# Performance work log

Hardware: AMD Instinct MI355X
Metric: run time of the kernel (lower is better)

## Reference

```python
import jax, jax.numpy as jnp
import numpy as np

B, CIN, H, W = 8, 128, 64, 64
COUT, KH, KW = 128, 3, 3
STRIDE = (1, 1)
PAD = (1, 1)
DIL = (1, 1)
GROUPS = 1
OFFSET_GROUPS = 1

def _out_size(i, k, s, p, d):
    return (i + 2 * p - d * (k - 1) - 1) // s + 1

HO = _out_size(H, KH, STRIDE[0], PAD[0], DIL[0])
WO = _out_size(W, KW, STRIDE[1], PAD[1], DIL[1])


def setup_inputs() -> dict:
    key = jax.random.key(0)
    k1, k2, k3, k4 = jax.random.split(key, 4)
    x = jax.random.normal(k1, (B, CIN, H, W), jnp.float32)
    offset = jax.random.normal(k2, (B, 2 * OFFSET_GROUPS * KH * KW, HO, WO), jnp.float32)
    fan_in = (CIN // GROUPS) * KH * KW
    bound = 1.0 / np.sqrt(fan_in)
    weight = jax.random.uniform(k3, (COUT, CIN // GROUPS, KH, KW), jnp.float32, -bound, bound)
    bias = jax.random.uniform(k4, (COUT,), jnp.float32, -bound, bound)
    return {"x": x, "offset": offset, "weight": weight, "bias": bias}


def _deform_conv2d(x, offset, weight, bias):
    Bn, Cin, Hi, Wi = x.shape
    K = KH * KW
    Goff, Gw = OFFSET_GROUPS, GROUPS
    Cpg = Cin // Goff

    # base sampling positions (before learned offsets)
    ys = jnp.arange(HO, dtype=jnp.float32) * STRIDE[0] - PAD[0]  # [HO]
    xs = jnp.arange(WO, dtype=jnp.float32) * STRIDE[1] - PAD[1]  # [WO]
    base_y = jnp.repeat(jnp.arange(KH, dtype=jnp.float32) * DIL[0], KW)  # [K]
    base_x = jnp.tile(jnp.arange(KW, dtype=jnp.float32) * DIL[1], KH)    # [K]

    # offsets: channel layout is 2*(g*K + k) + {0: dy, 1: dx}
    off = offset.reshape(Bn, Goff, K, 2, HO, WO)
    py = base_y[None, None, :, None, None] + ys[None, None, None, :, None] + off[:, :, :, 0]  # [B,Goff,K,HO,WO]
    px = base_x[None, None, :, None, None] + xs[None, None, None, None, :] + off[:, :, :, 1]

    y0 = jnp.floor(py)
    x0 = jnp.floor(px)
    ly = py - y0  # fractional weights
    lx = px - x0

    xg = x.reshape(Bn, Goff, Cpg, Hi * Wi)

    def gather_one(img, lin):  # img [Cpg, H*W], lin [K,HO,WO] -> [Cpg,K,HO,WO]
        return img[:, lin]

    gather = jax.vmap(jax.vmap(gather_one))  # over B and Goff

    def corner(yi, xi, w):
        # zero-padding semantics: out-of-bounds corner contributes 0
        mask = (yi >= 0) & (yi < Hi) & (xi >= 0) & (xi < Wi)
        iy = jnp.clip(yi, 0, Hi - 1).astype(jnp.int32)
        ix = jnp.clip(xi, 0, Wi - 1).astype(jnp.int32)
        lin = iy * Wi + ix  # [B,Goff,K,HO,WO]
        wm = (w * mask.astype(x.dtype))[:, :, None]  # broadcast over channel axis
        return gather(xg, lin) * wm  # [B,Goff,Cpg,K,HO,WO]

    val = (corner(y0, x0, (1 - ly) * (1 - lx))
           + corner(y0, x0 + 1, (1 - ly) * lx)
           + corner(y0 + 1, x0, ly * (1 - lx))
           + corner(y0 + 1, x0 + 1, ly * lx))  # [B,Goff,Cpg,K,HO,WO]

    # grouped conv accumulate
    val = val.reshape(Bn, Gw, Cin // Gw, K, HO, WO)
    wg = weight.reshape(Gw, COUT // Gw, Cin // Gw, K)
    out = jnp.einsum('bgckhw,gock->bgohw', val, wg).reshape(Bn, COUT, HO, WO)
    return out + bias[None, :, None, None]


def reference(x, offset, weight, bias):
    return _deform_conv2d(x, offset, weight, bias)
```

## Files before the change

### kernel.cpp

```cpp
#include <hip/hip_runtime.h>

typedef unsigned int   u32;
typedef unsigned short u16;
typedef short bf16x8 __attribute__((ext_vector_type(8)));
typedef float f32x4  __attribute__((ext_vector_type(4)));

#define CIN   128
#define COUT  128
#define Hh    64
#define Ww    64
#define Bb    8
#define KPOS  9
#define KDIM  (CIN*KPOS)
#define NKSTEP 36
#define XT_ELEMS (Bb*Hh*Ww*CIN)

__device__ __forceinline__ float bflo(u32 u){ return __uint_as_float(u << 16); }
__device__ __forceinline__ float bfhi(u32 u){ return __uint_as_float(u & 0xffff0000u); }

__device__ __forceinline__ u32 packbf(float a, float b){
    u32 ua = __float_as_uint(a);
    u32 ub = __float_as_uint(b);
    ua += 0x7fffu + ((ua >> 16) & 1u);
    ub += 0x7fffu + ((ub >> 16) & 1u);
    return (ua >> 16) | (ub & 0xffff0000u);
}
__device__ __forceinline__ u16 tobf(float a){
    u32 ua = __float_as_uint(a);
    ua += 0x7fffu + ((ua >> 16) & 1u);
    return (u16)(ua >> 16);
}

__global__ __launch_bounds__(256) void k_transpose(const float* __restrict__ x,
                                                   u16* __restrict__ xT){
    __shared__ float tile[32*33];
    int bi = blockIdx.x;
    int st = bi & 127, ct = (bi >> 7) & 3, b = bi >> 9;
    int sb = st * 32, cb = ct * 32;
    int tid = threadIdx.x;

    int i = tid >> 5, j = tid & 31;
    const float* xp = x + ((size_t)(b*CIN + cb) * 4096) + sb;
#pragma unroll
    for (int rr = 0; rr < 4; ++rr){
        int ci = i + rr*8;
        tile[ci*33 + j] = xp[(size_t)ci*4096 + j];
    }
    __syncthreads();

    int ii = tid >> 4, jj = tid & 15;
    u32* outp = (u32*)xT + ((size_t)b*4096 + sb)*64 + (cb >> 1) + jj;
#pragma unroll
    for (int rr = 0; rr < 2; ++rr){
        int sl = ii + rr*16;
        float v0 = tile[(2*jj  )*33 + sl];
        float v1 = tile[(2*jj+1)*33 + sl];
        outp[(size_t)sl*64] = packbf(v0, v1);
    }
}

__global__ __launch_bounds__(256) void k_wprep(const float* __restrict__ w,
                                               u16* __restrict__ Wt){
    int gid = blockIdx.x*256 + threadIdx.x;
    int jf   = gid & 7;
    int lane = (gid >> 3) & 63;
    int mt   = (gid >> 9) & 7;
    int kt   = gid >> 12;
    int m  = mt*16 + (lane & 15);
    int kk = (lane >> 4)*8 + jf;
    int ck = kt*32 + kk;
    int kpos = ck >> 7;
    int cin  = ck & 127;
    Wt[gid] = tobf(w[((size_t)m*128 + cin)*9 + kpos]);
}

__global__ __launch_bounds__(256, 1)
void k_main(const float* __restrict__ off, const float* __restrict__ bias,
            const u16* __restrict__ xT, const u16* __restrict__ Wt,
            float* __restrict__ out){
    __shared__ u32 Vsm[128*20];

    int tid = threadIdx.x;
    int bi  = blockIdx.x;
    int b   = bi & 7;
    int t   = bi >> 3;
    int s0  = t * 128;

    int p  = tid >> 1, hf = tid & 1;
    int ho = (s0 + p) >> 6;
    int wo = p & 63;
    const u16* xb_base = xT + (size_t)b * (Hh*Ww*CIN);

    int lane = tid & 63, wave = tid >> 6;
    int wm = wave >> 1, wn = wave & 1;
    int quad = lane >> 4, l16 = lane & 15;

    f32x4 acc[4][4];
#pragma unroll
    for (int i = 0; i < 4; ++i)
#pragma unroll
        for (int j = 0; j < 4; ++j) acc[i][j] = {0.f, 0.f, 0.f, 0.f};

    int   aa[4] = {0,0,0,0};
    float wt[4] = {0.f,0.f,0.f,0.f};

    for (int ks = 0; ks < NKSTEP; ++ks){
        uint4 araw[4];
#pragma unroll
        for (int i = 0; i < 4; ++i)
            araw[i] = *(const uint4*)(Wt + (size_t)(((ks*8 + wm*4 + i)*64 + lane))*8);

        if ((ks & 3) == 0){
            int kpos = ks >> 2;
            int kh = kpos / 3, kw = kpos - kh*3;
            size_t ob = ((size_t)(b*18 + 2*kpos))*4096 + (s0 + p);
            float dy = off[ob];
            float dx = off[ob + 4096];
            float py = (float)(ho + kh - 1) + dy;
            float px = (float)(wo + kw - 1) + dx;
            float y0f = floorf(py), x0f = floorf(px);
            float ly = py - y0f, lx = px - x0f;
            int y0 = (int)y0f, x0 = (int)x0f;
            int y1 = y0 + 1,  x1 = x0 + 1;
            float my0 = (y0 >= 0 && y0 < Hh) ? 1.f : 0.f;
            float my1 = (y1 >= 0 && y1 < Hh) ? 1.f : 0.f;
            float mx0 = (x0 >= 0 && x0 < Ww) ? 1.f : 0.f;
            float mx1 = (x1 >= 0 && x1 < Ww) ? 1.f : 0.f;
            float omly = 1.f - ly, omlx = 1.f - lx;
            wt[0] = omly*omlx*my0*mx0;
            wt[1] = omly*lx  *my0*mx1;
            wt[2] = ly  *omlx*my1*mx0;
            wt[3] = ly  *lx  *my1*mx1;
            int cy0 = min(max(y0,0),Hh-1), cy1 = min(max(y1,0),Hh-1);
            int cx0 = min(max(x0,0),Ww-1), cx1 = min(max(x1,0),Ww-1);
            aa[0] = (cy0*Ww + cx0)*CIN;
            aa[1] = (cy0*Ww + cx1)*CIN;
            aa[2] = (cy1*Ww + cx0)*CIN;
            aa[3] = (cy1*Ww + cx1)*CIN;
        }

        int coff = ((ks & 3) << 5) + hf*16;
        const u16* xb = xb_base + coff;
        uint4 q[4][2];
#pragma unroll
        for (int c = 0; c < 4; ++c){
            q[c][0] = *(const uint4*)(xb + aa[c]);
            q[c][1] = *(const uint4*)(xb + aa[c] + 8);
        }
        u32 res[8];
#pragma unroll
        for (int d = 0; d < 8; ++d){
            float lo = 0.f, hi = 0.f;
#pragma unroll
            for (int c = 0; c < 4; ++c){
                u32 u = ((const u32*)&q[c][0])[d];
                lo = fmaf(wt[c], bflo(u), lo);
                hi = fmaf(wt[c], bfhi(u), hi);
            }
            res[d] = packbf(lo, hi);
        }

        __syncthreads();
        u32* vrow = &Vsm[p*20 + hf*8];
        *(uint4*)(vrow    ) = *(uint4*)&res[0];
        *(uint4*)(vrow + 4) = *(uint4*)&res[4];
        __syncthreads();

        uint4 braw[4];
#pragma unroll
        for (int j = 0; j < 4; ++j)
            braw[j] = *(const uint4*)&Vsm[((wn*4 + j)*16 + l16)*20 + quad*4];
#pragma unroll
        for (int i = 0; i < 4; ++i){
            bf16x8 av = __builtin_bit_cast(bf16x8, araw[i]);
#pragma unroll
            for (int j = 0; j < 4; ++j){
                bf16x8 bv = __builtin_bit_cast(bf16x8, braw[j]);
                acc[i][j] = __builtin_amdgcn_mfma_f32_16x16x32_bf16(av, bv, acc[i][j], 0, 0, 0);
            }
        }
    }

#pragma unroll
    for (int i = 0; i < 4; ++i){
        int cout0 = (wm*4 + i)*16 + quad*4;
#pragma unroll
        for (int j = 0; j < 4; ++j){
            int pcol = (wn*4 + j)*16 + l16;
            size_t obase = ((size_t)(b*COUT + cout0))*4096 + (s0 + pcol);
#pragma unroll
            for (int r = 0; r < 4; ++r){
                out[obase + (size_t)r*4096] = acc[i][j][r] + bias[cout0 + r];
            }
        }
    }
}

extern "C" void kernel_launch(void* const* d_in, const int* in_sizes, int n_in,
                              void* d_out, int out_size, void* d_ws, size_t ws_size,
                              hipStream_t stream){
    const float* x    = (const float*)d_in[0];
    const float* off  = (const float*)d_in[1];
    const float* w    = (const float*)d_in[2];
    const float* bias = (const float*)d_in[3];
    float* out = (float*)d_out;

    u16* xT = (u16*)d_ws;
    u16* Wt = xT + XT_ELEMS;

    k_transpose<<<dim3(4096), dim3(256), 0, stream>>>(x, xT);
    k_wprep    <<<dim3(576),  dim3(256), 0, stream>>>(w, Wt);
    k_main     <<<dim3(256),  dim3(256), 0, stream>>>(off, bias, xT, Wt, out);
}
```

Before: 122.0 us.

## Halve spatial tile, double-buffer LDS, and prefetch next k-step gather

The main kernel now processes 64 output pixels per block instead of 128, which doubles the grid to 512 blocks and relaxes launch bounds to allow two blocks per CU. The im2col LDS buffer is double-buffered, and the next k-step's offset state, bilinear gather and weight fragments are loaded before the current step's MFMAs. This removes one barrier per step. The goal is better occupancy across the 256 CUs and overlap of gather latency with matrix math. In exchange, each block does half the MFMA work per weight-fragment load, so weight traffic from L2 doubles, and register pressure rises.

```diff
diff --git a/kernel.cpp b/kernel.cpp
--- a/kernel.cpp
+++ b/kernel.cpp
@@ -74,119 +74,137 @@
     Wt[gid] = tobf(w[((size_t)m*128 + cin)*9 + kpos]);
 }
 
-__global__ __launch_bounds__(256, 1)
+__global__ __launch_bounds__(256, 2)
 void k_main(const float* __restrict__ off, const float* __restrict__ bias,
             const u16* __restrict__ xT, const u16* __restrict__ Wt,
             float* __restrict__ out){
-    __shared__ u32 Vsm[128*20];
+    __shared__ u32 Vsm[2][64*20];
 
     int tid = threadIdx.x;
     int bi  = blockIdx.x;
     int b   = bi & 7;
     int t   = bi >> 3;
-    int s0  = t * 128;
-
-    int p  = tid >> 1, hf = tid & 1;
-    int ho = (s0 + p) >> 6;
-    int wo = p & 63;
+    int s0  = t * 64;
+
+    int p  = tid >> 2, qt = tid & 3;
+    int ho = t;
+    int wo = p;
     const u16* xb_base = xT + (size_t)b * (Hh*Ww*CIN);
 
     int lane = tid & 63, wave = tid >> 6;
     int wm = wave >> 1, wn = wave & 1;
     int quad = lane >> 4, l16 = lane & 15;
 
-    f32x4 acc[4][4];
+    f32x4 acc[4][2];
 #pragma unroll
     for (int i = 0; i < 4; ++i)
 #pragma unroll
-        for (int j = 0; j < 4; ++j) acc[i][j] = {0.f, 0.f, 0.f, 0.f};
-
-    int   aa[4] = {0,0,0,0};
-    float wt[4] = {0.f,0.f,0.f,0.f};
-
-    for (int ks = 0; ks < NKSTEP; ++ks){
-        uint4 araw[4];
+        for (int j = 0; j < 2; ++j) acc[i][j] = {0.f, 0.f, 0.f, 0.f};
+
+    int   aa[4];
+    float wt[4];
+
+    auto state = [&](int kpos){
+        int kh = kpos / 3, kw = kpos - kh*3;
+        size_t ob = ((size_t)(b*18 + 2*kpos))*4096 + (s0 + p);
+        float dy = off[ob];
+        float dx = off[ob + 4096];
+        float py = (float)(ho + kh - 1) + dy;
+        float px = (float)(wo + kw - 1) + dx;
+        float y0f = floorf(py), x0f = floorf(px);
+        float ly = py - y0f, lx = px - x0f;
+        int y0 = (int)y0f, x0 = (int)x0f;
+        int y1 = y0 + 1,  x1 = x0 + 1;
+        float my0 = (y0 >= 0 && y0 < Hh) ? 1.f : 0.f;
+        float my1 = (y1 >= 0 && y1 < Hh) ? 1.f : 0.f;
+        float mx0 = (x0 >= 0 && x0 < Ww) ? 1.f : 0.f;
+        float mx1 = (x1 >= 0 && x1 < Ww) ? 1.f : 0.f;
+        float omly = 1.f - ly, omlx = 1.f - lx;
+        wt[0] = omly*omlx*my0*mx0;
+        wt[1] = omly*lx  *my0*mx1;
+        wt[2] = ly  *omlx*my1*mx0;
+        wt[3] = ly  *lx  *my1*mx1;
+        int cy0 = min(max(y0,0),Hh-1), cy1 = min(max(y1,0),Hh-1);
+        int cx0 = min(max(x0,0),Ww-1), cx1 = min(max(x1,0),Ww-1);
+        aa[0] = (cy0*Ww + cx0)*CIN;
+        aa[1] = (cy0*Ww + cx1)*CIN;
+        aa[2] = (cy1*Ww + cx0)*CIN;
+        aa[3] = (cy1*Ww + cx1)*CIN;
+    };
+
+    auto gather = [&](int ks, uint4 q[4]){
+        int coff = ((ks & 3) << 5) + qt*8;
+        const u16* xb = xb_base + coff;
+#pragma unroll
+        for (int c = 0; c < 4; ++c)
+            q[c] = *(const uint4*)(xb + aa[c]);
+    };
+
+    auto loadA = [&](int ks, uint4 a[4]){
 #pragma unroll
         for (int i = 0; i < 4; ++i)
-            araw[i] = *(const uint4*)(Wt + (size_t)(((ks*8 + wm*4 + i)*64 + lane))*8);
-
-        if ((ks & 3) == 0){
-            int kpos = ks >> 2;
-            int kh = kpos / 3, kw = kpos - kh*3;
-            size_t ob = ((size_t)(b*18 + 2*kpos))*4096 + (s0 + p);
-            float dy = off[ob];
-            float dx = off[ob + 4096];
-            float py = (float)(ho + kh - 1) + dy;
-            float px = (float)(wo + kw - 1) + dx;
-            float y0f = floorf(py), x0f = floorf(px);
-            float ly = py - y0f, lx = px - x0f;
-            int y0 = (int)y0f, x0 = (int)x0f;
-            int y1 = y0 + 1,  x1 = x0 + 1;
-            float my0 = (y0 >= 0 && y0 < Hh) ? 1.f : 0.f;
-            float my1 = (y1 >= 0 && y1 < Hh) ? 1.f : 0.f;
-            float mx0 = (x0 >= 0 && x0 < Ww) ? 1.f : 0.f;
-            float mx1 = (x1 >= 0 && x1 < Ww) ? 1.f : 0.f;
-            float omly = 1.f - ly, omlx = 1.f - lx;
-            wt[0] = omly*omlx*my0*mx0;
-            wt[1] = omly*lx  *my0*mx1;
-            wt[2] = ly  *omlx*my1*mx0;
-            wt[3] = ly  *lx  *my1*mx1;
-            int cy0 = min(max(y0,0),Hh-1), cy1 = min(max(y1,0),Hh-1);
-            int cx0 = min(max(x0,0),Ww-1), cx1 = min(max(x1,0),Ww-1);
-            aa[0] = (cy0*Ww + cx0)*CIN;
-            aa[1] = (cy0*Ww + cx1)*CIN;
-            aa[2] = (cy1*Ww + cx0)*CIN;
-            aa[3] = (cy1*Ww + cx1)*CIN;
-        }
-
-        int coff = ((ks & 3) << 5) + hf*16;
-        const u16* xb = xb_base + coff;
-        uint4 q[4][2];
-#pragma unroll
-        for (int c = 0; c < 4; ++c){
-            q[c][0] = *(const uint4*)(xb + aa[c]);
-            q[c][1] = *(const uint4*)(xb + aa[c] + 8);
-        }
-        u32 res[8];
-#pragma unroll
-        for (int d = 0; d < 8; ++d){
+            a[i] = *(const uint4*)(Wt + (size_t)(((ks*8 + wm*4 + i)*64 + lane))*8);
+    };
+
+    auto blend_store = [&](const uint4 q[4], int buf){
+        u32 res[4];
+#pragma unroll
+        for (int d = 0; d < 4; ++d){
             float lo = 0.f, hi = 0.f;
 #pragma unroll
             for (int c = 0; c < 4; ++c){
-                u32 u = ((const u32*)&q[c][0])[d];
+                u32 u = ((const u32*)&q[0])[c*4 + d];
                 lo = fmaf(wt[c], bflo(u), lo);
                 hi = fmaf(wt[c], bfhi(u), hi);
             }
             res[d] = packbf(lo, hi);
         }
-
+        *(uint4*)&Vsm[buf][p*20 + qt*4] = *(uint4*)&res[0];
+    };
+
+    uint4 q[4], araw_cur[4], araw_nxt[4];
+    state(0);
+    gather(0, q);
+    loadA(0, araw_cur);
+    blend_store(q, 0);
+
+    for (int ks = 0; ks < NKSTEP; ++ks){
         __syncthreads();
-        u32* vrow = &Vsm[p*20 + hf*8];
-        *(uint4*)(vrow    ) = *(uint4*)&res[0];
-        *(uint4*)(vrow + 4) = *(uint4*)&res[4];
-        __syncthreads();
-
-        uint4 braw[4];
-#pragma unroll
-        for (int j = 0; j < 4; ++j)
-            braw[j] = *(const uint4*)&Vsm[((wn*4 + j)*16 + l16)*20 + quad*4];
+        int nxt = ks + 1;
+        bool have_nxt = (nxt < NKSTEP);
+        if (have_nxt){
+            if ((nxt & 3) == 0) state(nxt >> 2);
+            gather(nxt, q);
+            loadA(nxt, araw_nxt);
+        }
+
+        uint4 braw[2];
+#pragma unroll
+        for (int j = 0; j < 2; ++j)
+            braw[j] = *(const uint4*)&Vsm[ks & 1][((wn*2 + j)*16 + l16)*20 + quad*4];
 #pragma unroll
         for (int i = 0; i < 4; ++i){
-            bf16x8 av = __builtin_bit_cast(bf16x8, araw[i]);
-#pragma unroll
-            for (int j = 0; j < 4; ++j){
+            bf16x8 av = __builtin_bit_cast(bf16x8, araw_cur[i]);
+#pragma unroll
+            for (int j = 0; j < 2; ++j){
                 bf16x8 bv = __builtin_bit_cast(bf16x8, braw[j]);
                 acc[i][j] = __builtin_amdgcn_mfma_f32_16x16x32_bf16(av, bv, acc[i][j], 0, 0, 0);
             }
         }
+
+        if (have_nxt){
+            blend_store(q, nxt & 1);
+#pragma unroll
+            for (int i = 0; i < 4; ++i) araw_cur[i] = araw_nxt[i];
+        }
     }
 
 #pragma unroll
     for (int i = 0; i < 4; ++i){
         int cout0 = (wm*4 + i)*16 + quad*4;
 #pragma unroll
-        for (int j = 0; j < 4; ++j){
-            int pcol = (wn*4 + j)*16 + l16;
+        for (int j = 0; j < 2; ++j){
+            int pcol = (wn*2 + j)*16 + l16;
             size_t obase = ((size_t)(b*COUT + cout0))*4096 + (s0 + pcol);
 #pragma unroll
             for (int r = 0; r < 4; ++r){
@@ -210,5 +228,5 @@
 
     k_transpose<<<dim3(4096), dim3(256), 0, stream>>>(x, xT);
     k_wprep    <<<dim3(576),  dim3(256), 0, stream>>>(w, Wt);
-    k_main     <<<dim3(256),  dim3(256), 0, stream>>>(off, bias, xT, Wt, out);
-}
+    k_main     <<<dim3(512),  dim3(256), 0, stream>>>(off, bias, xT, Wt, out);
+}
```

After: 109.0 us. 1.12x faster.
